# Optimization experiments

Hardware: AMD Instinct MI355X
Metric: run time of the kernel (lower is better)

Reference implementation:

```python
import jax, jax.numpy as jnp
import numpy as np

BS, S, DIM, H = 4, 2048, 1024, 16
DH = DIM // H  # 64


def setup_inputs() -> dict:
    key = jax.random.key(0)
    ks = jax.random.split(key, 12)
    def lin(k, fan_in):
        bound = 1.0 / np.sqrt(fan_in)
        kw, kb = jax.random.split(k)
        W = jax.random.uniform(kw, (DIM, DIM), jnp.float32, -bound, bound)
        b = jax.random.uniform(kb, (DIM,), jnp.float32, -bound, bound)
        return W, b
    Wq, bq = lin(ks[0], DIM)
    Wk, bk = lin(ks[1], DIM)
    Wv, bv = lin(ks[2], DIM)
    Wo, bo = lin(ks[3], DIM)
    return {
        "query": jax.random.normal(ks[4], (BS, S, DIM), jnp.float32),
        "key": jax.random.normal(ks[5], (BS, S, DIM), jnp.float32),
        "value": jax.random.normal(ks[6], (BS, S, DIM), jnp.float32),
        "mask": jnp.ones((BS, S), jnp.int32),
        "Wq": Wq, "bq": bq, "Wk": Wk, "bk": bk,
        "Wv": Wv, "bv": bv, "Wo": Wo, "bo": bo,
    }


def reference(query, key, value, mask, Wq, bq, Wk, bk, Wv, bv, Wo, bo):
    bs, q_len, dim = query.shape
    def shape_heads(x):  # (bs, s, dim) -> (bs, H, s, DH)
        return x.reshape(bs, -1, H, DH).transpose(0, 2, 1, 3)
    # Linear projections (torch Linear: x @ W.T + b)
    q = shape_heads(query @ Wq.T + bq)
    k = shape_heads(key @ Wk.T + bk)
    v = shape_heads(value @ Wv.T + bv)
    q = q / jnp.sqrt(jnp.asarray(DH, q.dtype))
    # scores: (bs, H, q_len, k_len)
    scores = jnp.einsum('bhqd,bhkd->bhqk', q, k)
    neg = jnp.asarray(-jnp.inf, scores.dtype)
    pad = (mask == 0)[:, None, None, :]  # (bs,1,1,k_len)
    scores = jnp.where(pad, neg, scores)
    weights = jax.nn.softmax(scores, axis=-1)
    # dropout is identity in eval mode (reference is deterministic)
    context = jnp.einsum('bhqk,bhkd->bhqd', weights, v)
    context = context.transpose(0, 2, 1, 3).reshape(bs, q_len, dim)
    return context @ Wo.T + bo
```

## Files before the change

kernel.cpp:

```cpp
#include <hip/hip_runtime.h>
#include <hip/hip_bf16.h>
#include <math.h>

#define BSZ 4
#define SEQ 2048
#define DIMN 1024
#define NHEAD 16
#define DHEAD 64
#define MROWS (BSZ*SEQ)

typedef __bf16 bf16x8 __attribute__((ext_vector_type(8)));
typedef float  f32x4  __attribute__((ext_vector_type(4)));
typedef float  fvec4  __attribute__((ext_vector_type(4)));
typedef short  s16x4  __attribute__((ext_vector_type(4)));
typedef short  s16x8  __attribute__((ext_vector_type(8)));

__device__ __forceinline__ short f2bf(float v) {
  __hip_bfloat16 b = __float2bfloat16(v);
  return *reinterpret_cast<short*>(&b);
}
__device__ __forceinline__ float bf2f(short s) {
  __hip_bfloat16 b = *reinterpret_cast<__hip_bfloat16*>(&s);
  return __bfloat162float(b);
}

__device__ __forceinline__ void gld_lds16(const void* g, void* l) {
  __builtin_amdgcn_global_load_lds((const __attribute__((address_space(1))) void*)g,
                                   (__attribute__((address_space(3))) void*)l, 16, 0, 0);
}

#define QSC 0.18033688011112042f

__global__ __launch_bounds__(256) void pack_w4(
    const float* __restrict__ Wq, const float* __restrict__ Wk,
    const float* __restrict__ Wv, const float* __restrict__ Wo,
    short* __restrict__ WQh, short* __restrict__ WKh,
    short* __restrict__ WVh, short* __restrict__ WOh, short* __restrict__ WOl,
    long n)
{
  long i = ((long)blockIdx.x * 256 + threadIdx.x) * 4;
  if (i >= n) return;
  int which = blockIdx.y;
  if (which == 3) {
    fvec4 v = *(const fvec4*)&Wo[i];
    s16x4 h, l;
#pragma unroll
    for (int j = 0; j < 4; ++j) {
      short hb = f2bf(v[j]);
      h[j] = hb;
      l[j] = f2bf(v[j] - bf2f(hb));
    }
    *(s16x4*)&WOh[i] = h;
    *(s16x4*)&WOl[i] = l;
  } else {
    const float* src = which == 0 ? Wq : (which == 1 ? Wk : Wv);
    short* dst = which == 0 ? WQh : (which == 1 ? WKh : WVh);
    float sc = which == 0 ? QSC : 1.f;
    fvec4 v = *(const fvec4*)&src[i];
    s16x4 h;
#pragma unroll
    for (int j = 0; j < 4; ++j) h[j] = f2bf(v[j] * sc);
    *(s16x4*)&dst[i] = h;
  }
}

__global__ __launch_bounds__(256) void pack_hi3(
    const float* __restrict__ q, const float* __restrict__ k,
    const float* __restrict__ v,
    short* __restrict__ xq, short* __restrict__ xk, short* __restrict__ xv,
    long n)
{
  long i = ((long)blockIdx.x * 256 + threadIdx.x) * 4;
  if (i >= n) return;
  const float* src = blockIdx.y == 0 ? q : (blockIdx.y == 1 ? k : v);
  short* dst = blockIdx.y == 0 ? xq : (blockIdx.y == 1 ? xk : xv);
  fvec4 x = *(const fvec4*)&src[i];
  s16x4 h;
#pragma unroll
  for (int j = 0; j < 4; ++j) h[j] = f2bf(x[j]);
  *(s16x4*)&dst[i] = h;
}

__global__ __launch_bounds__(256) void maskbias_k(
    const int* __restrict__ mask, float* __restrict__ mb, int n)
{
  int i = blockIdx.x * 256 + threadIdx.x;
  if (i < n) mb[i] = mask[i] ? 0.f : -1e30f;
}

__global__ __launch_bounds__(64) void mask_flags(
    const int* __restrict__ mask, int* __restrict__ flg)
{
  int c = blockIdx.x;
  int base = (c >> 4) * SEQ + (c & 15) * 128;
  int m0 = mask[base + threadIdx.x];
  int m1 = mask[base + 64 + threadIdx.x];
  unsigned long long bal = __ballot(m0 != 0 && m1 != 0);
  if (threadIdx.x == 0) flg[c] = (bal == ~0ull) ? 1 : 0;
}

__global__ __launch_bounds__(256) void gemm_h(
    const short* __restrict__ A, const short* __restrict__ B,
    const float* __restrict__ bias, float bscale,
    float* __restrict__ Cf, short* __restrict__ Cb,
    int M, int N, int K, int mode)
{
  __shared__ __align__(16) short sA[128*32];
  __shared__ __align__(16) short sB[128*32];
  const int t = threadIdx.x;
  const int ln = t & 15, quad = (t & 63) >> 4, w = t >> 6;
  const int wm = w >> 1, wn = w & 1;
  const int m0 = blockIdx.y * 128, n0 = blockIdx.x * 128;
  const int lrow = t >> 2;
  const int lko = (((t & 3) ^ ((t >> 3) & 3))) * 8;
  const int fsw = ((ln >> 1) & 3);
  f32x4 acc[4][4];
#pragma unroll
  for (int i = 0; i < 4; ++i)
#pragma unroll
    for (int j = 0; j < 4; ++j) acc[i][j] = (f32x4){0.f,0.f,0.f,0.f};

  for (int k0 = 0; k0 < K; k0 += 32) {
    __syncthreads();
#pragma unroll
    for (int u = 0; u < 2; ++u) {
      int row = u*64 + lrow;
      gld_lds16(A + (size_t)(m0+row)*K + k0 + lko, sA + u*2048 + t*8);
      gld_lds16(B + (size_t)(n0+row)*K + k0 + lko, sB + u*2048 + t*8);
    }
    __syncthreads();
    bf16x8 af[4], bfr[4];
#pragma unroll
    for (int mt = 0; mt < 4; ++mt)
      af[mt] = *(bf16x8*)&sA[(wm*64 + mt*16 + ln)*32 + (quad ^ fsw)*8];
#pragma unroll
    for (int nt = 0; nt < 4; ++nt)
      bfr[nt] = *(bf16x8*)&sB[(wn*64 + nt*16 + ln)*32 + (quad ^ fsw)*8];
#pragma unroll
    for (int mt = 0; mt < 4; ++mt)
#pragma unroll
      for (int nt = 0; nt < 4; ++nt)
        acc[mt][nt] = __builtin_amdgcn_mfma_f32_16x16x32_bf16(af[mt], bfr[nt], acc[mt][nt], 0, 0, 0);
  }
#pragma unroll
  for (int nt = 0; nt < 4; ++nt) {
    int col = n0 + wn*64 + nt*16 + ln;
    float bv = bias[col] * bscale;
    if (mode == 2) {
      int hd = col >> 6, dd = col & 63;
#pragma unroll
      for (int mt = 0; mt < 4; ++mt) {
        int sg = m0 + wm*64 + mt*16 + quad*4;
        int b = sg >> 11, s = sg & 2047;
        s16x4 h;
#pragma unroll
        for (int r = 0; r < 4; ++r) h[r] = f2bf(acc[mt][nt][r] + bv);
        *(s16x4*)&Cb[((size_t)((b*16 + hd)*64 + dd))*SEQ + s] = h;
      }
    } else {
#pragma unroll
      for (int mt = 0; mt < 4; ++mt)
#pragma unroll
        for (int r = 0; r < 4; ++r) {
          int row = m0 + wm*64 + mt*16 + quad*4 + r;
          float val = acc[mt][nt][r] + bv;
          if (mode == 0) Cf[(size_t)row*N + col] = val;
          else           Cb[(size_t)row*N + col] = f2bf(val);
        }
    }
  }
}

__global__ __launch_bounds__(256) void gemm_sp(
    const short* __restrict__ Ah, const short* __restrict__ Al,
    const short* __restrict__ Bh, const short* __restrict__ Bl,
    const float* __restrict__ bias, float bscale,
    float* __restrict__ C, int M, int N, int K)
{
  __shared__ __align__(16) short sA[2*128*32];
  __shared__ __align__(16) short sB[2*128*32];
  const int t = threadIdx.x;
  const int ln = t & 15, quad = (t & 63) >> 4, w = t >> 6;
  const int wm = w >> 1, wn = w & 1;
  const int m0 = blockIdx.y * 128, n0 = blockIdx.x * 128;
  const int lrow = t >> 2;
  const int lko = (((t & 3) ^ ((t >> 3) & 3))) * 8;
  const int fsw = ((ln >> 1) & 3);
  f32x4 acc[4][4];
#pragma unroll
  for (int i = 0; i < 4; ++i)
#pragma unroll
    for (int j = 0; j < 4; ++j) acc[i][j] = (f32x4){0.f,0.f,0.f,0.f};

  for (int k0 = 0; k0 < K; k0 += 32) {
    __syncthreads();
#pragma unroll
    for (int u = 0; u < 2; ++u) {
      int row = u*64 + lrow;
      gld_lds16(Ah + (size_t)(m0+row)*K + k0 + lko, sA + u*2048 + t*8);
      gld_lds16(Al + (size_t)(m0+row)*K + k0 + lko, sA + 4096 + u*2048 + t*8);
      gld_lds16(Bh + (size_t)(n0+row)*K + k0 + lko, sB + u*2048 + t*8);
      gld_lds16(Bl + (size_t)(n0+row)*K + k0 + lko, sB + 4096 + u*2048 + t*8);
    }
    __syncthreads();
    bf16x8 ah[4], al[4], bh[4], bl[4];
#pragma unroll
    for (int mt = 0; mt < 4; ++mt) {
      int r = wm*64 + mt*16 + ln;
      ah[mt] = *(bf16x8*)&sA[r*32 + (quad ^ fsw)*8];
      al[mt] = *(bf16x8*)&sA[4096 + r*32 + (quad ^ fsw)*8];
    }
#pragma unroll
    for (int nt = 0; nt < 4; ++nt) {
      int r = wn*64 + nt*16 + ln;
      bh[nt] = *(bf16x8*)&sB[r*32 + (quad ^ fsw)*8];
      bl[nt] = *(bf16x8*)&sB[4096 + r*32 + (quad ^ fsw)*8];
    }
#pragma unroll
    for (int mt = 0; mt < 4; ++mt)
#pragma unroll
      for (int nt = 0; nt < 4; ++nt) {
        acc[mt][nt] = __builtin_amdgcn_mfma_f32_16x16x32_bf16(ah[mt], bh[nt], acc[mt][nt], 0, 0, 0);
        acc[mt][nt] = __builtin_amdgcn_mfma_f32_16x16x32_bf16(ah[mt], bl[nt], acc[mt][nt], 0, 0, 0);
        acc[mt][nt] = __builtin_amdgcn_mfma_f32_16x16x32_bf16(al[mt], bh[nt], acc[mt][nt], 0, 0, 0);
      }
  }
#pragma unroll
  for (int nt = 0; nt < 4; ++nt) {
    float bv = bias[n0 + wn*64 + nt*16 + ln] * bscale;
#pragma unroll
    for (int mt = 0; mt < 4; ++mt)
#pragma unroll
      for (int r = 0; r < 4; ++r)
        C[(size_t)(m0 + wm*64 + mt*16 + quad*4 + r)*N + (n0 + wn*64 + nt*16 + ln)] =
            acc[mt][nt][r] + bv;
  }
}

__global__ __launch_bounds__(256, 2) void attn_sp3(
    const short* __restrict__ QB, const short* __restrict__ KB,
    const short* __restrict__ VT, const float* __restrict__ mb,
    const int* __restrict__ flg,
    short* __restrict__ CTXh, short* __restrict__ CTXl)
{
  __shared__ __align__(16) short lds[32768];
  short* sK = lds;
  short* sV = lds + 8192;
  short* sP = lds + 16384;
  short* sQ = lds + 16384;

  const int t = threadIdx.x;
  const int ln = t & 15, quad = (t & 63) >> 4, w = t >> 6;
  const int g = blockIdx.x;
  const int chunk = g >> 3, qt128 = chunk & 15, bh = ((chunk >> 4) << 3) + (g & 7);
  const int b = bh >> 4, hd = bh & 15;
  const int fsw = ((ln >> 1) & 3);

#pragma unroll
  for (int i = 0; i < 4; ++i) {
    int unit = i*256 + t;
    int ks = unit >> 9, idx = unit & 511, row = idx >> 2, c = idx & 3;
    int sw = (c ^ ((row >> 1) & 3)) * 8;
    gld_lds16(QB + (size_t)(b*SEQ + qt128*128 + row)*DIMN + hd*64 + ks*32 + sw,
              sQ + unit*8);
  }
  __syncthreads();
  bf16x8 qf[2][2];
#pragma unroll
  for (int qt = 0; qt < 2; ++qt)
#pragma unroll
    for (int ks = 0; ks < 2; ++ks) {
      int q = w*32 + qt*16 + ln;
      qf[qt][ks] = *(bf16x8*)&sQ[ks*4096 + q*32 + (quad ^ fsw)*8];
    }

  f32x4 o_acc[2][4];
#pragma unroll
  for (int qt = 0; qt < 2; ++qt)
#pragma unroll
    for (int nt = 0; nt < 4; ++nt) o_acc[qt][nt] = (f32x4){0.f,0.f,0.f,0.f};
  float m_run[2] = {-1e30f, -1e30f}, l_run[2] = {0.f, 0.f};

  for (int kt = 0; kt < SEQ/128; ++kt) {
    __syncthreads();
#pragma unroll
    for (int i = 0; i < 4; ++i) {
      int unit = i*256 + t;
      { int ks = unit >> 9, idx = unit & 511, row = idx >> 2, c = idx & 3;
        int sw = (c ^ ((row >> 1) & 3)) * 8;
        gld_lds16(KB + (size_t)(b*SEQ + kt*128 + row)*DIMN + hd*64 + ks*32 + sw,
                  sK + unit*8); }
      { int ksv = unit >> 8, idx = unit & 255, d = idx >> 2, c = idx & 3;
        int sw = (c ^ ((d >> 1) & 3)) * 8;
        gld_lds16(VT + ((size_t)bh*64 + d)*SEQ + kt*128 + ksv*32 + sw,
                  sV + unit*8); }
    }
    __syncthreads();

    f32x4 sacc[8][2];
#pragma unroll
    for (int mt = 0; mt < 8; ++mt)
#pragma unroll
      for (int qt = 0; qt < 2; ++qt) sacc[mt][qt] = (f32x4){0.f,0.f,0.f,0.f};
#pragma unroll
    for (int ks = 0; ks < 2; ++ks)
#pragma unroll
      for (int mt = 0; mt < 8; ++mt) {
        bf16x8 kf = *(bf16x8*)&sK[ks*4096 + (mt*16 + ln)*32 + (quad ^ fsw)*8];
        sacc[mt][0] = __builtin_amdgcn_mfma_f32_16x16x32_bf16(kf, qf[0][ks], sacc[mt][0], 0, 0, 0);
        sacc[mt][1] = __builtin_amdgcn_mfma_f32_16x16x32_bf16(kf, qf[1][ks], sacc[mt][1], 0, 0, 0);
      }

    bool allv = flg[b*16 + kt] != 0;
    if (!allv) {
#pragma unroll
      for (int mt = 0; mt < 8; ++mt) {
        fvec4 m4 = *(const fvec4*)&mb[b*SEQ + kt*128 + mt*16 + quad*4];
#pragma unroll
        for (int qt = 0; qt < 2; ++qt)
#pragma unroll
          for (int r = 0; r < 4; ++r) sacc[mt][qt][r] += m4[r];
      }
    }

    float alpha[2];
#pragma unroll
    for (int qt = 0; qt < 2; ++qt) {
      float tmax = -1e30f;
#pragma unroll
      for (int mt = 0; mt < 8; ++mt)
#pragma unroll
        for (int r = 0; r < 4; ++r) tmax = fmaxf(tmax, sacc[mt][qt][r]);
      tmax = fmaxf(tmax, __shfl_xor(tmax, 16));
      tmax = fmaxf(tmax, __shfl_xor(tmax, 32));
      float mnew = fmaxf(m_run[qt], tmax);
      alpha[qt] = exp2f(m_run[qt] - mnew);
      m_run[qt] = mnew;
      float rs = 0.f;
      const int q = w*32 + qt*16 + ln;
#pragma unroll
      for (int mt = 0; mt < 8; ++mt) {
        s16x4 ph;
#pragma unroll
        for (int r = 0; r < 4; ++r) {
          float p = exp2f(sacc[mt][qt][r] - mnew);
          rs += p;
          ph[r] = f2bf(p);
        }
        int phys = (mt*2 + (quad >> 1)) ^ ln;
        *(s16x4*)&sP[q*128 + phys*8 + (quad & 1)*4] = ph;
      }
      rs += __shfl_xor(rs, 16);
      rs += __shfl_xor(rs, 32);
      l_run[qt] = l_run[qt]*alpha[qt] + rs;
    }

#pragma unroll
    for (int qt = 0; qt < 2; ++qt) {
      float a4[4];
#pragma unroll
      for (int r = 0; r < 4; ++r) a4[r] = __shfl(alpha[qt], quad*4 + r);
#pragma unroll
      for (int nt = 0; nt < 4; ++nt)
#pragma unroll
        for (int r = 0; r < 4; ++r) o_acc[qt][nt][r] *= a4[r];
    }

#pragma unroll
    for (int ksv = 0; ksv < 4; ++ksv) {
      bf16x8 vf[4];
#pragma unroll
      for (int nt = 0; nt < 4; ++nt)
        vf[nt] = *(bf16x8*)&sV[ksv*2048 + (nt*16 + ln)*32 + (quad ^ fsw)*8];
#pragma unroll
      for (int qt = 0; qt < 2; ++qt) {
        const int q = w*32 + qt*16 + ln;
        bf16x8 pf = *(bf16x8*)&sP[q*128 + ((ksv*4 + quad) ^ ln)*8];
#pragma unroll
        for (int nt = 0; nt < 4; ++nt)
          o_acc[qt][nt] = __builtin_amdgcn_mfma_f32_16x16x32_bf16(pf, vf[nt], o_acc[qt][nt], 0, 0, 0);
      }
    }
  }

#pragma unroll
  for (int qt = 0; qt < 2; ++qt) {
    float invl = (l_run[qt] > 0.f) ? 1.f / l_run[qt] : 0.f;
    float i4[4];
#pragma unroll
    for (int r = 0; r < 4; ++r) i4[r] = __shfl(invl, quad*4 + r);
#pragma unroll
    for (int nt = 0; nt < 4; ++nt)
#pragma unroll
      for (int r = 0; r < 4; ++r) {
        int qrow = qt128*128 + w*32 + qt*16 + quad*4 + r;
        size_t idx = (size_t)(b*SEQ + qrow)*DIMN + hd*64 + nt*16 + ln;
        float val = o_acc[qt][nt][r] * i4[r];
        short hb = f2bf(val);
        CTXh[idx] = hb;
        CTXl[idx] = f2bf(val - bf2f(hb));
      }
  }
}

__global__ __launch_bounds__(256) void gemm_bt(
    const float* __restrict__ X, const float* __restrict__ W,
    const float* __restrict__ bias, float* __restrict__ C,
    int M, int N, int K)
{
  __shared__ __align__(16) float Xs[16][68];
  __shared__ __align__(16) float Ws[16][68];
  const int t  = threadIdx.x;
  const int tx = t & 15, ty = t >> 4;
  const int m0 = blockIdx.y << 6, n0 = blockIdx.x << 6;
  const int ldr = t >> 2;
  const int lk  = (t & 3) << 2;
  float acc[4][4] = {{0.f}};
  const float* Xp = X + (size_t)(m0 + ldr) * K + lk;
  const float* Wp = W + (size_t)(n0 + ldr) * K + lk;
  for (int k0 = 0; k0 < K; k0 += 16) {
    float4 xa = *(const float4*)(Xp + k0);
    float4 wa = *(const float4*)(Wp + k0);
    Xs[lk+0][ldr]=xa.x; Xs[lk+1][ldr]=xa.y; Xs[lk+2][ldr]=xa.z; Xs[lk+3][ldr]=xa.w;
    Ws[lk+0][ldr]=wa.x; Ws[lk+1][ldr]=wa.y; Ws[lk+2][ldr]=wa.z; Ws[lk+3][ldr]=wa.w;
    __syncthreads();
#pragma unroll
    for (int kk = 0; kk < 16; ++kk) {
      float4 a4 = *(const float4*)&Xs[kk][ty<<2];
      float4 b4 = *(const float4*)&Ws[kk][tx<<2];
      float av[4] = {a4.x, a4.y, a4.z, a4.w};
      float bv[4] = {b4.x, b4.y, b4.z, b4.w};
#pragma unroll
      for (int i = 0; i < 4; ++i)
#pragma unroll
        for (int j = 0; j < 4; ++j)
          acc[i][j] = fmaf(av[i], bv[j], acc[i][j]);
    }
    __syncthreads();
  }
  float4 bb4 = *(const float4*)&bias[n0 + (tx<<2)];
  const float bv[4] = {bb4.x, bb4.y, bb4.z, bb4.w};
#pragma unroll
  for (int i = 0; i < 4; ++i) {
    float4 o;
    o.x = acc[i][0]+bv[0]; o.y = acc[i][1]+bv[1];
    o.z = acc[i][2]+bv[2]; o.w = acc[i][3]+bv[3];
    *(float4*)&C[(size_t)(m0 + (ty<<2) + i) * N + n0 + (tx<<2)] = o;
  }
}

__global__ __launch_bounds__(256) void attn_fwd(
    const float* __restrict__ Q, const float* __restrict__ Kbuf,
    const float* __restrict__ Vbuf, const int* __restrict__ mask,
    float* __restrict__ CTX)
{
  __shared__ __align__(16) float Qs[64][68];
  __shared__ __align__(16) float KPs[64][68];
  __shared__ __align__(16) float Vs[64][68];
  const int t  = threadIdx.x;
  const int tx = t & 15, ty = t >> 4;
  const int qt = blockIdx.x;
  const int bh = blockIdx.y;
  const int b  = bh >> 4, h = bh & 15;
  const int ldr = t >> 2;
  const int lcb = (t & 3) << 2;
  const float* Qp = Q + (size_t)(b*SEQ + (qt<<6)) * DIMN + h*DHEAD;
#pragma unroll
  for (int u = 0; u < 4; ++u) {
    int kb = lcb + (u<<4);
    float4 q4 = *(const float4*)(Qp + (size_t)ldr*DIMN + kb);
    Qs[kb+0][ldr]=q4.x; Qs[kb+1][ldr]=q4.y; Qs[kb+2][ldr]=q4.z; Qs[kb+3][ldr]=q4.w;
  }
  float mrow[4], lsum[4], o[4][4];
#pragma unroll
  for (int i = 0; i < 4; ++i) {
    mrow[i] = -1e30f; lsum[i] = 0.f;
#pragma unroll
    for (int j = 0; j < 4; ++j) o[i][j] = 0.f;
  }
  const int qrow0 = ty << 2;
  const int col0  = tx << 2;
  for (int kt = 0; kt < SEQ/64; ++kt) {
    __syncthreads();
    const float* Kp = Kbuf + (size_t)(b*SEQ + (kt<<6)) * DIMN + h*DHEAD;
    const float* Vp = Vbuf + (size_t)(b*SEQ + (kt<<6)) * DIMN + h*DHEAD;
#pragma unroll
    for (int u = 0; u < 4; ++u) {
      int kb = lcb + (u<<4);
      float4 k4 = *(const float4*)(Kp + (size_t)ldr*DIMN + kb);
      KPs[kb+0][ldr]=k4.x; KPs[kb+1][ldr]=k4.y; KPs[kb+2][ldr]=k4.z; KPs[kb+3][ldr]=k4.w;
      float4 v4 = *(const float4*)(Vp + (size_t)ldr*DIMN + kb);
      *(float4*)&Vs[ldr][kb] = v4;
    }
    __syncthreads();
    float s[4][4] = {{0.f}};
#pragma unroll 8
    for (int kk = 0; kk < 64; ++kk) {
      float4 a4 = *(const float4*)&Qs[kk][qrow0];
      float4 b4 = *(const float4*)&KPs[kk][col0];
      float av[4] = {a4.x, a4.y, a4.z, a4.w};
      float bv[4] = {b4.x, b4.y, b4.z, b4.w};
#pragma unroll
      for (int i = 0; i < 4; ++i)
#pragma unroll
        for (int j = 0; j < 4; ++j)
          s[i][j] = fmaf(av[i], bv[j], s[i][j]);
    }
    int mk[4];
#pragma unroll
    for (int j = 0; j < 4; ++j) mk[j] = mask[b*SEQ + (kt<<6) + col0 + j];
    float p[4][4];
#pragma unroll
    for (int i = 0; i < 4; ++i) {
#pragma unroll
      for (int j = 0; j < 4; ++j)
        s[i][j] = mk[j] ? s[i][j]*0.125f : -1e30f;
      float tm = fmaxf(fmaxf(s[i][0], s[i][1]), fmaxf(s[i][2], s[i][3]));
#pragma unroll
      for (int off = 8; off >= 1; off >>= 1)
        tm = fmaxf(tm, __shfl_xor(tm, off, 64));
      float mnew  = fmaxf(mrow[i], tm);
      float aa = __expf(mrow[i] - mnew);
      mrow[i] = mnew;
      float rsum = 0.f;
#pragma unroll
      for (int j = 0; j < 4; ++j) {
        float pv = __expf(s[i][j] - mnew);
        p[i][j] = pv; rsum += pv;
      }
#pragma unroll
      for (int off = 8; off >= 1; off >>= 1)
        rsum += __shfl_xor(rsum, off, 64);
      lsum[i] = lsum[i]*aa + rsum;
#pragma unroll
      for (int j = 0; j < 4; ++j) o[i][j] *= aa;
    }
    __syncthreads();
#pragma unroll
    for (int i = 0; i < 4; ++i)
#pragma unroll
      for (int j = 0; j < 4; ++j)
        KPs[col0 + j][qrow0 + i] = p[i][j];
    __syncthreads();
#pragma unroll 8
    for (int kk = 0; kk < 64; ++kk) {
      float4 a4 = *(const float4*)&KPs[kk][qrow0];
      float4 v4 = *(const float4*)&Vs[kk][col0];
      float av[4] = {a4.x, a4.y, a4.z, a4.w};
      float vv[4] = {v4.x, v4.y, v4.z, v4.w};
#pragma unroll
      for (int i = 0; i < 4; ++i)
#pragma unroll
        for (int j = 0; j < 4; ++j)
          o[i][j] = fmaf(av[i], vv[j], o[i][j]);
    }
  }
  float* Cp = CTX + (size_t)(b*SEQ + (qt<<6)) * DIMN + h*DHEAD;
#pragma unroll
  for (int i = 0; i < 4; ++i) {
    float inv = lsum[i] > 0.f ? 1.0f/lsum[i] : 0.f;
    float4 ov;
    ov.x = o[i][0]*inv; ov.y = o[i][1]*inv;
    ov.z = o[i][2]*inv; ov.w = o[i][3]*inv;
    *(float4*)(Cp + (size_t)(qrow0 + i)*DIMN + col0) = ov;
  }
}

extern "C" void kernel_launch(void* const* d_in, const int* in_sizes, int n_in,
                              void* d_out, int out_size, void* d_ws, size_t ws_size,
                              hipStream_t stream)
{
  const float* query = (const float*)d_in[0];
  const float* key   = (const float*)d_in[1];
  const float* value = (const float*)d_in[2];
  const int*   mask  = (const int*)d_in[3];
  const float* Wq = (const float*)d_in[4];
  const float* bq = (const float*)d_in[5];
  const float* Wk = (const float*)d_in[6];
  const float* bk = (const float*)d_in[7];
  const float* Wv = (const float*)d_in[8];
  const float* bv = (const float*)d_in[9];
  const float* Wo = (const float*)d_in[10];
  const float* bo = (const float*)d_in[11];
  float* out = (float*)d_out;

  const size_t E  = (size_t)MROWS * DIMN;
  const size_t WE = (size_t)DIMN * DIMN;

  const size_t o_XB   = 5*WE*2;
  const size_t o_QB   = o_XB   + 3*E*2;
  const size_t o_KB   = o_QB   + E*2;
  const size_t o_VT   = o_KB   + E*2;
  const size_t o_CTXh = o_VT   + E*2;
  const size_t o_CTXl = o_CTXh + E*2;
  const size_t o_MB   = o_CTXl + E*2;
  const size_t o_FLG  = o_MB   + MROWS*4;
  const size_t NEED   = o_FLG  + 64*4;

  if (ws_size < NEED) {
    const size_t n = E;
    float* Qb = (float*)d_ws;
    float* Kb = Qb + n;
    float* Vb = Kb + n;
    float* Cb = Vb + n;
    dim3 gg(DIMN/64, MROWS/64), blk(256);
    hipLaunchKernelGGL(gemm_bt, gg, blk, 0, stream, query, Wq, bq, Qb, MROWS, DIMN, DIMN);
    hipLaunchKernelGGL(gemm_bt, gg, blk, 0, stream, key,   Wk, bk, Kb, MROWS, DIMN, DIMN);
    hipLaunchKernelGGL(gemm_bt, gg, blk, 0, stream, value, Wv, bv, Vb, MROWS, DIMN, DIMN);
    dim3 ga(SEQ/64, BSZ*NHEAD);
    hipLaunchKernelGGL(attn_fwd, ga, blk, 0, stream, Qb, Kb, Vb, mask, Cb);
    hipLaunchKernelGGL(gemm_bt, gg, blk, 0, stream, Cb, Wo, bo, out, MROWS, DIMN, DIMN);
    return;
  }

  char* Wp = (char*)d_ws;
  short* WQh = (short*)Wp;
  short* WKh = WQh + WE;
  short* WVh = WQh + 2*WE;
  short* WOh = WQh + 3*WE;
  short* WOl = WQh + 4*WE;
  short* XBq  = (short*)(Wp + o_XB);
  short* XBk  = XBq + E;
  short* XBv  = XBk + E;
  short* QB   = (short*)(Wp + o_QB);
  short* KB   = (short*)(Wp + o_KB);
  short* VT   = (short*)(Wp + o_VT);
  short* CTXh = (short*)(Wp + o_CTXh);
  short* CTXl = (short*)(Wp + o_CTXl);
  float* MB   = (float*)(Wp + o_MB);
  int*   FLG  = (int*)(Wp + o_FLG);

  dim3 blk(256);
  dim3 gW(WE/1024, 4), gX(E/1024, 3);
  dim3 gg(DIMN/128, MROWS/128);
  dim3 gat(BSZ*NHEAD*SEQ/128);

  hipLaunchKernelGGL(pack_w4, gW, blk, 0, stream, Wq, Wk, Wv, Wo,
                     WQh, WKh, WVh, WOh, WOl, (long)WE);
  hipLaunchKernelGGL(maskbias_k, dim3(MROWS/256), blk, 0, stream, mask, MB, MROWS);
  hipLaunchKernelGGL(mask_flags, dim3(64), dim3(64), 0, stream, mask, FLG);
  hipLaunchKernelGGL(pack_hi3, gX, blk, 0, stream, query, key, value,
                     XBq, XBk, XBv, (long)E);

  hipLaunchKernelGGL(gemm_h, gg, blk, 0, stream, XBq, WQh, bq, QSC,
                     (float*)nullptr, QB, MROWS, DIMN, DIMN, 1);
  hipLaunchKernelGGL(gemm_h, gg, blk, 0, stream, XBk, WKh, bk, 1.f,
                     (float*)nullptr, KB, MROWS, DIMN, DIMN, 1);
  hipLaunchKernelGGL(gemm_h, gg, blk, 0, stream, XBv, WVh, bv, 1.f,
                     (float*)nullptr, VT, MROWS, DIMN, DIMN, 2);

  hipLaunchKernelGGL(attn_sp3, gat, blk, 0, stream, QB, KB, VT, MB, FLG, CTXh, CTXl);

  hipLaunchKernelGGL(gemm_sp, gg, blk, 0, stream, CTXh, CTXl, WOh, WOl, bo, 1.f,
                     out, MROWS, DIMN, DIMN);
}
```

Before: 458.9 us.

## Rewrite attention with 32x32 MFMA, register-resident P, and lazy rescaling

Replaces the 16x16x32 MFMA flash-attention kernel with one built on 32x32x16 MFMA. Each wave now owns 32 query rows, and the P tile stays in registers: it is converted with v_cvt_pk_bf16_f32 and rearranged with v_permlane32_swap instead of round-tripping through LDS. That halves LDS use and allows raising the occupancy hint to 3 blocks. It also skips rescaling the O accumulator unless the running max grows by more than a threshold, which cuts exp and multiply work. The cost is higher register pressure from the 16-wide accumulators, plus a small numerical risk from the deferred max update.

Result: faster. 433.5 us (-5.5%).

```diff
diff --git a/kernel.cpp b/kernel.cpp
--- a/kernel.cpp
+++ b/kernel.cpp
@@ -11,6 +11,7 @@
 
 typedef __bf16 bf16x8 __attribute__((ext_vector_type(8)));
 typedef float  f32x4  __attribute__((ext_vector_type(4)));
+typedef float  f32x16 __attribute__((ext_vector_type(16)));
 typedef float  fvec4  __attribute__((ext_vector_type(4)));
 typedef short  s16x4  __attribute__((ext_vector_type(4)));
 typedef short  s16x8  __attribute__((ext_vector_type(8)));
@@ -237,170 +238,145 @@
   }
 }
 
-__global__ __launch_bounds__(256, 2) void attn_sp3(
+__global__ __launch_bounds__(256, 3) void attn_32(
     const short* __restrict__ QB, const short* __restrict__ KB,
     const short* __restrict__ VT, const float* __restrict__ mb,
     const int* __restrict__ flg,
     short* __restrict__ CTXh, short* __restrict__ CTXl)
 {
-  __shared__ __align__(16) short lds[32768];
+  __shared__ __align__(16) short lds[16384];
   short* sK = lds;
   short* sV = lds + 8192;
-  short* sP = lds + 16384;
-  short* sQ = lds + 16384;
 
   const int t = threadIdx.x;
-  const int ln = t & 15, quad = (t & 63) >> 4, w = t >> 6;
-  const int g = blockIdx.x;
-  const int chunk = g >> 3, qt128 = chunk & 15, bh = ((chunk >> 4) << 3) + (g & 7);
+  const int l31 = t & 31, hi = (t >> 5) & 1, w = t >> 6;
+  const int gb = blockIdx.x;
+  const int chunk = gb >> 3, qt128 = chunk & 15, bh = ((chunk >> 4) << 3) + (gb & 7);
   const int b = bh >> 4, hd = bh & 15;
-  const int fsw = ((ln >> 1) & 3);
 
 #pragma unroll
   for (int i = 0; i < 4; ++i) {
-    int unit = i*256 + t;
-    int ks = unit >> 9, idx = unit & 511, row = idx >> 2, c = idx & 3;
-    int sw = (c ^ ((row >> 1) & 3)) * 8;
-    gld_lds16(QB + (size_t)(b*SEQ + qt128*128 + row)*DIMN + hd*64 + ks*32 + sw,
-              sQ + unit*8);
+    int u = i*256 + t;
+    int row = u >> 3, gr = (u & 7) ^ (row & 7);
+    gld_lds16(QB + ((size_t)(b*SEQ + qt128*128 + row))*DIMN + hd*64 + gr*8,
+              sK + u*8);
   }
   __syncthreads();
-  bf16x8 qf[2][2];
-#pragma unroll
-  for (int qt = 0; qt < 2; ++qt)
-#pragma unroll
-    for (int ks = 0; ks < 2; ++ks) {
-      int q = w*32 + qt*16 + ln;
-      qf[qt][ks] = *(bf16x8*)&sQ[ks*4096 + q*32 + (quad ^ fsw)*8];
-    }
-
-  f32x4 o_acc[2][4];
-#pragma unroll
-  for (int qt = 0; qt < 2; ++qt)
-#pragma unroll
-    for (int nt = 0; nt < 4; ++nt) o_acc[qt][nt] = (f32x4){0.f,0.f,0.f,0.f};
-  float m_run[2] = {-1e30f, -1e30f}, l_run[2] = {0.f, 0.f};
+  const int q = w*32 + l31;
+  bf16x8 qf[4];
+#pragma unroll
+  for (int ks = 0; ks < 4; ++ks)
+    qf[ks] = *(bf16x8*)&sK[q*64 + ((ks*2 + hi) ^ (q & 7))*8];
+
+  f32x16 o_acc[2] = {};
+  float m_run = -1e30f, l_run = 0.f;
 
   for (int kt = 0; kt < SEQ/128; ++kt) {
     __syncthreads();
 #pragma unroll
     for (int i = 0; i < 4; ++i) {
-      int unit = i*256 + t;
-      { int ks = unit >> 9, idx = unit & 511, row = idx >> 2, c = idx & 3;
-        int sw = (c ^ ((row >> 1) & 3)) * 8;
-        gld_lds16(KB + (size_t)(b*SEQ + kt*128 + row)*DIMN + hd*64 + ks*32 + sw,
-                  sK + unit*8); }
-      { int ksv = unit >> 8, idx = unit & 255, d = idx >> 2, c = idx & 3;
-        int sw = (c ^ ((d >> 1) & 3)) * 8;
-        gld_lds16(VT + ((size_t)bh*64 + d)*SEQ + kt*128 + ksv*32 + sw,
-                  sV + unit*8); }
-    }
-    __syncthreads();
-
-    f32x4 sacc[8][2];
-#pragma unroll
-    for (int mt = 0; mt < 8; ++mt)
-#pragma unroll
-      for (int qt = 0; qt < 2; ++qt) sacc[mt][qt] = (f32x4){0.f,0.f,0.f,0.f};
-#pragma unroll
-    for (int ks = 0; ks < 2; ++ks)
-#pragma unroll
-      for (int mt = 0; mt < 8; ++mt) {
-        bf16x8 kf = *(bf16x8*)&sK[ks*4096 + (mt*16 + ln)*32 + (quad ^ fsw)*8];
-        sacc[mt][0] = __builtin_amdgcn_mfma_f32_16x16x32_bf16(kf, qf[0][ks], sacc[mt][0], 0, 0, 0);
-        sacc[mt][1] = __builtin_amdgcn_mfma_f32_16x16x32_bf16(kf, qf[1][ks], sacc[mt][1], 0, 0, 0);
-      }
-
-    bool allv = flg[b*16 + kt] != 0;
-    if (!allv) {
-#pragma unroll
-      for (int mt = 0; mt < 8; ++mt) {
-        fvec4 m4 = *(const fvec4*)&mb[b*SEQ + kt*128 + mt*16 + quad*4];
-#pragma unroll
-        for (int qt = 0; qt < 2; ++qt)
-#pragma unroll
-          for (int r = 0; r < 4; ++r) sacc[mt][qt][r] += m4[r];
-      }
-    }
-
-    float alpha[2];
-#pragma unroll
-    for (int qt = 0; qt < 2; ++qt) {
-      float tmax = -1e30f;
-#pragma unroll
-      for (int mt = 0; mt < 8; ++mt)
-#pragma unroll
-        for (int r = 0; r < 4; ++r) tmax = fmaxf(tmax, sacc[mt][qt][r]);
-      tmax = fmaxf(tmax, __shfl_xor(tmax, 16));
-      tmax = fmaxf(tmax, __shfl_xor(tmax, 32));
-      float mnew = fmaxf(m_run[qt], tmax);
-      alpha[qt] = exp2f(m_run[qt] - mnew);
-      m_run[qt] = mnew;
-      float rs = 0.f;
-      const int q = w*32 + qt*16 + ln;
-#pragma unroll
-      for (int mt = 0; mt < 8; ++mt) {
-        s16x4 ph;
-#pragma unroll
-        for (int r = 0; r < 4; ++r) {
-          float p = exp2f(sacc[mt][qt][r] - mnew);
-          rs += p;
-          ph[r] = f2bf(p);
+      int u = i*256 + t;
+      { int row = u >> 3, gr = (u & 7) ^ (row & 7);
+        gld_lds16(KB + ((size_t)(b*SEQ + kt*128 + row))*DIMN + hd*64 + gr*8,
+                  sK + u*8); }
+      { int d = u >> 4, gr = (u & 15) ^ (d & 15);
+        gld_lds16(VT + ((size_t)(bh*64 + d))*SEQ + kt*128 + gr*8,
+                  sV + u*8); }
+    }
+    __syncthreads();
+
+    f32x16 sacc[4] = {};
+#pragma unroll
+    for (int ks = 0; ks < 4; ++ks)
+#pragma unroll
+      for (int mt = 0; mt < 4; ++mt) {
+        int kc = mt*32 + l31;
+        bf16x8 kf = *(bf16x8*)&sK[kc*64 + ((ks*2 + hi) ^ (kc & 7))*8];
+        sacc[mt] = __builtin_amdgcn_mfma_f32_32x32x16_bf16(kf, qf[ks], sacc[mt], 0, 0, 0);
+      }
+
+    if (!flg[b*16 + kt]) {
+#pragma unroll
+      for (int mt = 0; mt < 4; ++mt)
+#pragma unroll
+        for (int r = 0; r < 16; ++r)
+          sacc[mt][r] += mb[b*SEQ + kt*128 + mt*32 + (r&3) + 8*(r>>2) + 4*hi];
+    }
+
+    float tmax = -1e30f;
+#pragma unroll
+    for (int mt = 0; mt < 4; ++mt)
+#pragma unroll
+      for (int r = 0; r < 16; ++r) tmax = fmaxf(tmax, sacc[mt][r]);
+    tmax = fmaxf(tmax, __shfl_xor(tmax, 32));
+
+    if (!__all(tmax <= m_run + 8.f)) {
+      float mnew = fmaxf(m_run, tmax);
+      float alpha = exp2f(m_run - mnew);
+      l_run *= alpha;
+#pragma unroll
+      for (int dt = 0; dt < 2; ++dt)
+#pragma unroll
+        for (int r = 0; r < 16; ++r) o_acc[dt][r] *= alpha;
+      m_run = mnew;
+    }
+
+    float rs = 0.f;
+#pragma unroll
+    for (int mt = 0; mt < 4; ++mt)
+#pragma unroll
+      for (int r = 0; r < 16; ++r) {
+        float p = exp2f(sacc[mt][r] - m_run);
+        sacc[mt][r] = p;
+        rs += p;
+      }
+    rs += __shfl_xor(rs, 32);
+    l_run += rs;
+
+#pragma unroll
+    for (int mt = 0; mt < 4; ++mt) {
+      unsigned wv[8];
+#pragma unroll
+      for (int i = 0; i < 8; ++i) {
+        float plo = sacc[mt][2*i], phi = sacc[mt][2*i+1];
+        asm("v_cvt_pk_bf16_f32 %0, %1, %2" : "=v"(wv[i]) : "v"(plo), "v"(phi));
+      }
+#pragma unroll
+      for (int h = 0; h < 2; ++h) {
+        unsigned f0 = wv[h*4+0], f1 = wv[h*4+1], f2 = wv[h*4+2], f3 = wv[h*4+3];
+        asm volatile("v_permlane32_swap_b32 %0, %1" : "+v"(f0), "+v"(f2));
+        asm volatile("v_permlane32_swap_b32 %0, %1" : "+v"(f1), "+v"(f3));
+        union { unsigned u[4]; bf16x8 v; } pu;
+        pu.u[0] = f0; pu.u[1] = f1; pu.u[2] = f2; pu.u[3] = f3;
+        const int kcs = mt*2 + h;
+#pragma unroll
+        for (int dt = 0; dt < 2; ++dt) {
+          int d = dt*32 + l31;
+          bf16x8 vf = *(bf16x8*)&sV[d*128 + ((kcs*2 + hi) ^ (d & 15))*8];
+          o_acc[dt] = __builtin_amdgcn_mfma_f32_32x32x16_bf16(vf, pu.v, o_acc[dt], 0, 0, 0);
         }
-        int phys = (mt*2 + (quad >> 1)) ^ ln;
-        *(s16x4*)&sP[q*128 + phys*8 + (quad & 1)*4] = ph;
-      }
-      rs += __shfl_xor(rs, 16);
-      rs += __shfl_xor(rs, 32);
-      l_run[qt] = l_run[qt]*alpha[qt] + rs;
-    }
-
-#pragma unroll
-    for (int qt = 0; qt < 2; ++qt) {
-      float a4[4];
-#pragma unroll
-      for (int r = 0; r < 4; ++r) a4[r] = __shfl(alpha[qt], quad*4 + r);
-#pragma unroll
-      for (int nt = 0; nt < 4; ++nt)
-#pragma unroll
-        for (int r = 0; r < 4; ++r) o_acc[qt][nt][r] *= a4[r];
-    }
-
-#pragma unroll
-    for (int ksv = 0; ksv < 4; ++ksv) {
-      bf16x8 vf[4];
-#pragma unroll
-      for (int nt = 0; nt < 4; ++nt)
-        vf[nt] = *(bf16x8*)&sV[ksv*2048 + (nt*16 + ln)*32 + (quad ^ fsw)*8];
-#pragma unroll
-      for (int qt = 0; qt < 2; ++qt) {
-        const int q = w*32 + qt*16 + ln;
-        bf16x8 pf = *(bf16x8*)&sP[q*128 + ((ksv*4 + quad) ^ ln)*8];
-#pragma unroll
-        for (int nt = 0; nt < 4; ++nt)
-          o_acc[qt][nt] = __builtin_amdgcn_mfma_f32_16x16x32_bf16(pf, vf[nt], o_acc[qt][nt], 0, 0, 0);
-      }
-    }
-  }
-
-#pragma unroll
-  for (int qt = 0; qt < 2; ++qt) {
-    float invl = (l_run[qt] > 0.f) ? 1.f / l_run[qt] : 0.f;
-    float i4[4];
-#pragma unroll
-    for (int r = 0; r < 4; ++r) i4[r] = __shfl(invl, quad*4 + r);
-#pragma unroll
-    for (int nt = 0; nt < 4; ++nt)
-#pragma unroll
-      for (int r = 0; r < 4; ++r) {
-        int qrow = qt128*128 + w*32 + qt*16 + quad*4 + r;
-        size_t idx = (size_t)(b*SEQ + qrow)*DIMN + hd*64 + nt*16 + ln;
-        float val = o_acc[qt][nt][r] * i4[r];
+      }
+    }
+  }
+
+  float invl = (l_run > 0.f) ? 1.f / l_run : 0.f;
+  const size_t rowbase = (size_t)(b*SEQ + qt128*128 + q)*DIMN + hd*64;
+#pragma unroll
+  for (int dt = 0; dt < 2; ++dt)
+#pragma unroll
+    for (int rg = 0; rg < 4; ++rg) {
+      s16x4 hq, lq;
+#pragma unroll
+      for (int r2 = 0; r2 < 4; ++r2) {
+        float val = o_acc[dt][rg*4 + r2] * invl;
         short hb = f2bf(val);
-        CTXh[idx] = hb;
-        CTXl[idx] = f2bf(val - bf2f(hb));
-      }
-  }
+        hq[r2] = hb;
+        lq[r2] = f2bf(val - bf2f(hb));
+      }
+      size_t idx = rowbase + dt*32 + rg*8 + hi*4;
+      *(s16x4*)&CTXh[idx] = hq;
+      *(s16x4*)&CTXl[idx] = lq;
+    }
 }
 
 __global__ __launch_bounds__(256) void gemm_bt(
@@ -649,7 +625,7 @@
   hipLaunchKernelGGL(gemm_h, gg, blk, 0, stream, XBv, WVh, bv, 1.f,
                      (float*)nullptr, VT, MROWS, DIMN, DIMN, 2);
 
-  hipLaunchKernelGGL(attn_sp3, gat, blk, 0, stream, QB, KB, VT, MB, FLG, CTXh, CTXl);
+  hipLaunchKernelGGL(attn_32, gat, blk, 0, stream, QB, KB, VT, MB, FLG, CTXh, CTXl);
 
   hipLaunchKernelGGL(gemm_sp, gg, blk, 0, stream, CTXh, CTXl, WOh, WOl, bo, 1.f,
                      out, MROWS, DIMN, DIMN);
```
